# Kernel tuning notes

Measured on AMD Instinct MI355X. Metric: run time of the kernel, lower is better.

## Reference

```python
import jax, jax.numpy as jnp
import numpy as np

B, S, D_IN = 2, 2048, 1024
EMBED, HEADS = 1024, 16
HEAD_DIM = EMBED // HEADS

def setup_inputs() -> dict:
    key = jax.random.key(0)
    k1, k2, k3 = jax.random.split(key, 3)
    # xavier_uniform bounds
    def xavier(k, shape):
        fan_in, fan_out = shape[1], shape[0]
        lim = jnp.sqrt(6.0 / (fan_in + fan_out))
        return jax.random.uniform(k, shape, jnp.float32, -lim, lim)
    x = jax.random.normal(k1, (B, S, D_IN), jnp.float32)
    qkv_w = xavier(k2, (3 * EMBED, D_IN))   # torch Linear weight layout [out, in]
    qkv_b = jnp.zeros((3 * EMBED,), jnp.float32)
    o_w = xavier(k3, (EMBED, EMBED))
    o_b = jnp.zeros((EMBED,), jnp.float32)
    return {"x": x, "qkv_w": qkv_w, "qkv_b": qkv_b, "o_w": o_w, "o_b": o_b}

def reference(x, qkv_w, qkv_b, o_w, o_b):
    Bq, Sq, _ = x.shape
    qkv = x @ qkv_w.T + qkv_b                       # [B,S,3E]
    qkv = qkv.reshape(Bq, Sq, HEADS, 3 * HEAD_DIM).transpose(0, 2, 1, 3)  # [B,H,S,3d]
    q, k, v = jnp.split(qkv, 3, axis=-1)            # each [B,H,S,d]
    scale = 1.0 / jnp.sqrt(jnp.asarray(HEAD_DIM, x.dtype))
    logits = jnp.einsum('bhqd,bhkd->bhqk', q, k) * scale
    attn = jax.nn.softmax(logits, axis=-1)
    vals = jnp.einsum('bhqk,bhkd->bhqd', attn, v)   # [B,H,S,d]
    vals = vals.transpose(0, 2, 1, 3).reshape(Bq, Sq, EMBED)
    return vals @ o_w.T + o_b
```

## Files before the change

kernel.cpp:

```cpp
#include <hip/hip_runtime.h>
#include <hip/hip_bf16.h>

#define B_    2
#define S_    2048
#define DIN   1024
#define EMB   1024
#define NH    16
#define HD    64
#define N3    3072
#define MROWS 4096
#define KVB   64
#define QBLK  128

typedef short bf16x8 __attribute__((ext_vector_type(8)));
typedef float f32x4  __attribute__((ext_vector_type(4)));
typedef unsigned short u16;
typedef u16 u16x8 __attribute__((ext_vector_type(8)));
typedef u16 u16x4 __attribute__((ext_vector_type(4)));
typedef unsigned int u32;

__device__ __forceinline__ u16 f2bf(float f) {
  union { float f; unsigned u; } x; x.f = f;
  unsigned r = x.u + 0x7fffu + ((x.u >> 16) & 1u);
  return (u16)(r >> 16);
}

__device__ __forceinline__ u32 cvtpk(float lo, float hi) {
  u32 r;
  asm("v_cvt_pk_bf16_f32 %0, %1, %2" : "=v"(r) : "v"(lo), "v"(hi));
  return r;
}

__device__ __forceinline__ void gload16(const void* g, void* l) {
  __builtin_amdgcn_global_load_lds(
      (const __attribute__((address_space(1))) unsigned int*)g,
      (__attribute__((address_space(3))) unsigned int*)l, 16, 0, 0);
}

__global__ void cast4(const float* __restrict__ in, u16* __restrict__ out, int n4) {
  const int i = blockIdx.x * 256 + threadIdx.x;
  if (i < n4) {
    const float4 v = ((const float4*)in)[i];
    u16x4 o;
    o[0] = f2bf(v.x); o[1] = f2bf(v.y); o[2] = f2bf(v.z); o[3] = f2bf(v.w);
    ((u16x4*)out)[i] = o;
  }
}

template<int EPI>
__global__ __launch_bounds__(256)
void gemm_bt(const u16* __restrict__ A, const u16* __restrict__ W,
             const float* __restrict__ bias, float* __restrict__ Cf,
             u16* __restrict__ Qb, u16* __restrict__ Kb, u16* __restrict__ VbT,
             int M, int N, int K) {
  __shared__ u16 Als[128 * 32];
  __shared__ u16 Bls[128 * 32];
  const int tid  = threadIdx.x;
  const int wave = tid >> 6, lane = tid & 63;
  const int lhi  = lane >> 4, llo = lane & 15;
  const int wr   = wave >> 1, wc = wave & 1;
  const int m0   = blockIdx.y * 128, n0 = blockIdx.x * 128;

  const f32x4 fzero = {0.f, 0.f, 0.f, 0.f};
  f32x4 acc[4][4];
#pragma unroll
  for (int m = 0; m < 4; ++m)
#pragma unroll
    for (int n = 0; n < 4; ++n) acc[m][n] = fzero;

  for (int k0 = 0; k0 < K; k0 += 32) {
#pragma unroll
    for (int i = 0; i < 2; ++i) {
      const int e   = (tid + i * 256) * 8;
      const int row = e >> 5, col = e & 31;
      gload16(A + (size_t)(m0 + row) * K + k0 + col, (char*)Als + wave * 1024 + i * 4096);
      gload16(W + (size_t)(n0 + row) * K + k0 + col, (char*)Bls + wave * 1024 + i * 4096);
    }
    __syncthreads();
    bf16x8 af[4], bfr[4];
#pragma unroll
    for (int m = 0; m < 4; ++m) af[m]  = *(const bf16x8*)&Als[(wr * 64 + m * 16 + llo) * 32 + lhi * 8];
#pragma unroll
    for (int n = 0; n < 4; ++n) bfr[n] = *(const bf16x8*)&Bls[(wc * 64 + n * 16 + llo) * 32 + lhi * 8];
#pragma unroll
    for (int m = 0; m < 4; ++m)
#pragma unroll
      for (int n = 0; n < 4; ++n)
        acc[m][n] = __builtin_amdgcn_mfma_f32_16x16x32_bf16(af[m], bfr[n], acc[m][n], 0, 0, 0);
    __syncthreads();
  }

#pragma unroll
  for (int n = 0; n < 4; ++n) {
    const int colb = n0 + wc * 64 + n * 16;
    const int gcol = colb + llo;
    const float bv = bias[gcol];
    if (EPI == 0) {
      const int h   = colb / 192;
      const int rr  = colb - h * 192;
      const int sec = rr >> 6;
      const int d   = (rr & 63) + llo;
#pragma unroll
      for (int m = 0; m < 4; ++m) {
        const int rowb = m0 + wr * 64 + m * 16 + lhi * 4;
        const int b = rowb >> 11, s0 = rowb & 2047;
        if (sec == 2) {
          u16x4 vv;
#pragma unroll
          for (int r = 0; r < 4; ++r) vv[r] = f2bf(acc[m][n][r] + bv);
          *(u16x4*)&VbT[((size_t)(b * NH + h) * HD + d) * S_ + s0] = vv;
        } else {
          u16* dst = (sec == 0) ? Qb : Kb;
          const float scl = (sec == 0) ? 0.18033688f : 1.0f;
#pragma unroll
          for (int r = 0; r < 4; ++r)
            dst[(((size_t)(b * NH + h) * S_ + s0 + r) << 6) + d] = f2bf((acc[m][n][r] + bv) * scl);
        }
      }
    } else {
#pragma unroll
      for (int m = 0; m < 4; ++m) {
        const int rowb = m0 + wr * 64 + m * 16 + lhi * 4;
#pragma unroll
        for (int r = 0; r < 4; ++r)
          Cf[(size_t)(rowb + r) * N + gcol] = acc[m][n][r] + bv;
      }
    }
  }
}

__global__ __launch_bounds__(512)
void attn_fwd(const u16* __restrict__ Qb, const u16* __restrict__ Kb,
              const u16* __restrict__ VbT, u16* __restrict__ Obf) {
  __shared__ __align__(16) u16 Kls[2][KVB * HD];
  __shared__ __align__(16) u16 Vls[2][HD * KVB];
  const int tid  = threadIdx.x;
  const int wave = tid >> 6, lane = tid & 63;
  const int lhi  = lane >> 4, llo = lane & 15;
  const int bh   = blockIdx.y;
  const int q0   = blockIdx.x * QBLK;
  const size_t base  = (size_t)bh * S_ * HD;
  const size_t basev = (size_t)bh * HD * S_;

  bf16x8 qf[2];
#pragma unroll
  for (int kk = 0; kk < 2; ++kk)
    qf[kk] = *(const bf16x8*)&Qb[base + (size_t)(q0 + wave * 16 + llo) * HD + kk * 32 + lhi * 8];

  const int srow  = tid >> 3;
  const int xslot = (tid & 7) ^ (srow & 7);
  const u16* kSrc = Kb  + base  + (size_t)srow * HD + xslot * 8;
  const u16* vSrc = VbT + basev + (size_t)srow * S_ + xslot * 8;
  const int ldsOff = wave * 1024;

  const int ro  = llo * 128;
  const int sw0 = ((((0 * 4 + lhi) ^ (llo & 7)) << 4)) + ro;
  const int sw1 = ((((1 * 4 + lhi) ^ (llo & 7)) << 4)) + ro;

  const f32x4 fzero = {0.f, 0.f, 0.f, 0.f};
  f32x4 o[4];
#pragma unroll
  for (int jd = 0; jd < 4; ++jd) o[jd] = fzero;
  float mrow = -1e30f, lsum = 0.f;

  gload16(kSrc, (char*)Kls[0] + ldsOff);
  gload16(vSrc, (char*)Vls[0] + ldsOff);
  __syncthreads();

  int cur = 0;
  for (int t = 0; t < S_ / KVB; ++t) {
    if (t + 1 < S_ / KVB) {
      gload16(kSrc + (size_t)(t + 1) * KVB * HD, (char*)Kls[cur ^ 1] + ldsOff);
      gload16(vSrc + (t + 1) * KVB,              (char*)Vls[cur ^ 1] + ldsOff);
    }
    const char* Kt = (const char*)Kls[cur];
    const char* Vt = (const char*)Vls[cur];

    f32x4 s[4];
#pragma unroll
    for (int j = 0; j < 4; ++j) s[j] = fzero;
    __builtin_amdgcn_s_setprio(1);
#pragma unroll
    for (int j = 0; j < 4; ++j) {
      bf16x8 k0 = *(const bf16x8*)(Kt + sw0 + j * 2048);
      bf16x8 k1 = *(const bf16x8*)(Kt + sw1 + j * 2048);
      s[j] = __builtin_amdgcn_mfma_f32_16x16x32_bf16(k0, qf[0], s[j], 0, 0, 0);
      s[j] = __builtin_amdgcn_mfma_f32_16x16x32_bf16(k1, qf[1], s[j], 0, 0, 0);
    }
    __builtin_amdgcn_s_setprio(0);

    float tmax = -1e30f;
#pragma unroll
    for (int j = 0; j < 4; ++j)
#pragma unroll
      for (int r = 0; r < 4; ++r) tmax = fmaxf(tmax, s[j][r]);
    tmax = fmaxf(tmax, __shfl_xor(tmax, 16));
    tmax = fmaxf(tmax, __shfl_xor(tmax, 32));
    const float mnew  = fmaxf(mrow, tmax);
    const float alpha = exp2f(mrow - mnew);
    float tsum = 0.f;
    u32 dwp[4][2];
#pragma unroll
    for (int j = 0; j < 4; ++j) {
      const float p0 = exp2f(s[j][0] - mnew), p1 = exp2f(s[j][1] - mnew);
      const float p2 = exp2f(s[j][2] - mnew), p3 = exp2f(s[j][3] - mnew);
      tsum += (p0 + p1) + (p2 + p3);
      dwp[j][0] = cvtpk(p0, p1);
      dwp[j][1] = cvtpk(p2, p3);
    }
    tsum += __shfl_xor(tsum, 16);
    tsum += __shfl_xor(tsum, 32);
    lsum = lsum * alpha + tsum;
    mrow = mnew;

    const int l0 = llo + ((lhi & 1) << 5);
    const int l1 = l0 + 16;
    const bool hi = (lhi & 2) != 0;
    bf16x8 pf[2];
#pragma unroll
    for (int kk = 0; kk < 2; ++kk) {
      const u32 a0 = __shfl(dwp[kk * 2][0], l0),     a1 = __shfl(dwp[kk * 2][1], l0);
      const u32 b0 = __shfl(dwp[kk * 2 + 1][0], l0), b1 = __shfl(dwp[kk * 2 + 1][1], l0);
      const u32 c0 = __shfl(dwp[kk * 2][0], l1),     c1 = __shfl(dwp[kk * 2][1], l1);
      const u32 d0 = __shfl(dwp[kk * 2 + 1][0], l1), d1 = __shfl(dwp[kk * 2 + 1][1], l1);
      union { u32 u[4]; bf16x8 v; } P;
      P.u[0] = hi ? b0 : a0;  P.u[1] = hi ? b1 : a1;
      P.u[2] = hi ? d0 : c0;  P.u[3] = hi ? d1 : c1;
      pf[kk] = P.v;
    }

#pragma unroll
    for (int r = 0; r < 4; ++r) {
      const float f = __shfl(alpha, lhi * 4 + r);
#pragma unroll
      for (int jd = 0; jd < 4; ++jd) o[jd][r] *= f;
    }

    __builtin_amdgcn_s_setprio(1);
#pragma unroll
    for (int jd = 0; jd < 4; ++jd) {
      bf16x8 v0 = *(const bf16x8*)(Vt + sw0 + jd * 2048);
      bf16x8 v1 = *(const bf16x8*)(Vt + sw1 + jd * 2048);
      o[jd] = __builtin_amdgcn_mfma_f32_16x16x32_bf16(pf[0], v0, o[jd], 0, 0, 0);
      o[jd] = __builtin_amdgcn_mfma_f32_16x16x32_bf16(pf[1], v1, o[jd], 0, 0, 0);
    }
    __builtin_amdgcn_s_setprio(0);

    __syncthreads();
    cur ^= 1;
  }

  const float li = 1.0f / lsum;
  const int b = bh >> 4, h = bh & 15;
#pragma unroll
  for (int r = 0; r < 4; ++r) {
    const float f = __shfl(li, lhi * 4 + r);
    const int q = q0 + wave * 16 + lhi * 4 + r;
    u16* dst = Obf + ((size_t)(b * S_ + q) * NH + h) * HD;
#pragma unroll
    for (int jd = 0; jd < 4; ++jd)
      dst[jd * 16 + llo] = f2bf(o[jd][r] * f);
  }
}

extern "C" void kernel_launch(void* const* d_in, const int* in_sizes, int n_in,
                              void* d_out, int out_size, void* d_ws, size_t ws_size,
                              hipStream_t stream) {
  const float* x     = (const float*)d_in[0];
  const float* qkv_w = (const float*)d_in[1];
  const float* qkv_b = (const float*)d_in[2];
  const float* o_w   = (const float*)d_in[3];
  const float* o_b   = (const float*)d_in[4];
  float* out = (float*)d_out;

  char* ws = (char*)d_ws;
  u16* xbf  = (u16*)(ws);
  u16* wqkv = (u16*)(ws + (8u  << 20));
  u16* wo   = (u16*)(ws + (14u << 20));
  u16* Qb   = (u16*)(ws + (16u << 20));
  u16* Kb   = (u16*)(ws + (24u << 20));
  u16* VbT  = (u16*)(ws + (32u << 20));
  u16* atnb = xbf;

  cast4<<<4096, 256, 0, stream>>>(x,     xbf,  1048576);
  cast4<<<3072, 256, 0, stream>>>(qkv_w, wqkv,  786432);
  cast4<<<1024, 256, 0, stream>>>(o_w,   wo,    262144);

  gemm_bt<0><<<dim3(N3 / 128, MROWS / 128), 256, 0, stream>>>(
      xbf, wqkv, qkv_b, nullptr, Qb, Kb, VbT, MROWS, N3, DIN);

  attn_fwd<<<dim3(S_ / QBLK, B_ * NH), 512, 0, stream>>>(Qb, Kb, VbT, atnb);

  gemm_bt<1><<<dim3(EMB / 128, MROWS / 128), 256, 0, stream>>>(
      atnb, wo, o_b, out, nullptr, nullptr, nullptr, MROWS, EMB, EMB);
}
```

Baseline: 160.8 us.

## Deepen attention K/V prefetch to four-stage ring with explicit vmcnt waits

Replaces the double-buffered K/V LDS pipeline with a four-slot ring that keeps three tiles in flight. It uses manual s_waitcnt vmcnt counts and raw s_barrier in place of __syncthreads, so global-to-LDS loads overlap more compute and the full drain at every iteration goes away. It also reorders the row-max reduction into a tree. LDS use doubles, which can lower occupancy. The hand-counted vmcnt values assume each gload16 issues exactly one memory op per call, so correctness depends on that.

```diff
diff --git a/kernel.cpp b/kernel.cpp
--- a/kernel.cpp
+++ b/kernel.cpp
@@ -11,6 +11,7 @@
 #define MROWS 4096
 #define KVB   64
 #define QBLK  128
+#define NT    (S_ / KVB)
 
 typedef short bf16x8 __attribute__((ext_vector_type(8)));
 typedef float f32x4  __attribute__((ext_vector_type(4)));
@@ -132,8 +133,8 @@
 __global__ __launch_bounds__(512)
 void attn_fwd(const u16* __restrict__ Qb, const u16* __restrict__ Kb,
               const u16* __restrict__ VbT, u16* __restrict__ Obf) {
-  __shared__ __align__(16) u16 Kls[2][KVB * HD];
-  __shared__ __align__(16) u16 Vls[2][HD * KVB];
+  __shared__ __align__(16) u16 Kls[4][KVB * HD];
+  __shared__ __align__(16) u16 Vls[4][HD * KVB];
   const int tid  = threadIdx.x;
   const int wave = tid >> 6, lane = tid & 63;
   const int lhi  = lane >> 4, llo = lane & 15;
@@ -163,18 +164,14 @@
   for (int jd = 0; jd < 4; ++jd) o[jd] = fzero;
   float mrow = -1e30f, lsum = 0.f;
 
-  gload16(kSrc, (char*)Kls[0] + ldsOff);
-  gload16(vSrc, (char*)Vls[0] + ldsOff);
-  __syncthreads();
-
-  int cur = 0;
-  for (int t = 0; t < S_ / KVB; ++t) {
-    if (t + 1 < S_ / KVB) {
-      gload16(kSrc + (size_t)(t + 1) * KVB * HD, (char*)Kls[cur ^ 1] + ldsOff);
-      gload16(vSrc + (t + 1) * KVB,              (char*)Vls[cur ^ 1] + ldsOff);
-    }
-    const char* Kt = (const char*)Kls[cur];
-    const char* Vt = (const char*)Vls[cur];
+  auto issue = [&](int t) {
+    gload16(kSrc + (size_t)t * KVB * HD, (char*)Kls[t & 3] + ldsOff);
+    gload16(vSrc + t * KVB,              (char*)Vls[t & 3] + ldsOff);
+  };
+
+  auto compute = [&](int t) {
+    const char* Kt = (const char*)Kls[t & 3];
+    const char* Vt = (const char*)Vls[t & 3];
 
     f32x4 s[4];
 #pragma unroll
@@ -191,9 +188,10 @@
 
     float tmax = -1e30f;
 #pragma unroll
-    for (int j = 0; j < 4; ++j)
-#pragma unroll
-      for (int r = 0; r < 4; ++r) tmax = fmaxf(tmax, s[j][r]);
+    for (int j = 0; j < 4; ++j) {
+      const float a = fmaxf(s[j][0], s[j][1]), b = fmaxf(s[j][2], s[j][3]);
+      tmax = fmaxf(tmax, fmaxf(a, b));
+    }
     tmax = fmaxf(tmax, __shfl_xor(tmax, 16));
     tmax = fmaxf(tmax, __shfl_xor(tmax, 32));
     const float mnew  = fmaxf(mrow, tmax);
@@ -245,10 +243,27 @@
       o[jd] = __builtin_amdgcn_mfma_f32_16x16x32_bf16(pf[1], v1, o[jd], 0, 0, 0);
     }
     __builtin_amdgcn_s_setprio(0);
-
-    __syncthreads();
-    cur ^= 1;
-  }
+  };
+
+  issue(0); issue(1); issue(2);
+
+#define BAR() do { asm volatile("" ::: "memory"); \
+                   __builtin_amdgcn_s_barrier();  \
+                   asm volatile("" ::: "memory"); } while (0)
+  for (int t = 0; t < NT - 3; ++t) {
+    issue(t + 3);
+    asm volatile("s_waitcnt vmcnt(6)" ::: "memory");
+    BAR();
+    compute(t);
+    BAR();
+  }
+  asm volatile("s_waitcnt vmcnt(4)" ::: "memory");
+  BAR(); compute(NT - 3); BAR();
+  asm volatile("s_waitcnt vmcnt(2)" ::: "memory");
+  BAR(); compute(NT - 2); BAR();
+  asm volatile("s_waitcnt vmcnt(0)" ::: "memory");
+  BAR(); compute(NT - 1);
+#undef BAR
 
   const float li = 1.0f / lsum;
   const int b = bh >> 4, h = bh & 15;
```

Measured after the change: 163.5 us. Within noise of the previous version (+1.7%).
